# Performance work log

Hardware: AMD Instinct MI355X
Metric: run time of the kernel (lower is better)

## Reference

```python
import jax, jax.numpy as jnp
import numpy as np

T, D, H, V, Z = 32, 128, 256, 32000, 256


def _gru_cell(x, h, W_ih, W_hh, b_ih, b_hh):
    # PyTorch GRU cell, gate order r,z,n. x,h: [D,H]
    gi = x @ W_ih.T + b_ih
    gh = h @ W_hh.T + b_hh
    i_r, i_z, i_n = jnp.split(gi, 3, axis=-1)
    h_r, h_z, h_n = jnp.split(gh, 3, axis=-1)
    r = jax.nn.sigmoid(i_r + h_r)
    z = jax.nn.sigmoid(i_z + h_z)
    n = jnp.tanh(i_n + r * h_n)
    return (1.0 - z) * n + z * h


def _tree_rnn(nodes, edges, h0, emb, pc, ps):
    # nodes/edges: [T,D]; h0: [D,H]. Child vs sibling GRU chosen per-node by edges.
    def step(h, te):
        tok, e = te
        x = emb[tok]                       # [D,H]
        hc = _gru_cell(x, h, *pc)
        hs = _gru_cell(x, h, *ps)
        hn = jnp.where(e[:, None], hc, hs)  # branch-aware state update
        return hn, hn                       # seq_len=1, L=1 => output == new state
    h_final, outs = jax.lax.scan(step, h0, (nodes, edges))
    return outs, h_final                    # outs: [T,D,H]


def setup_inputs() -> dict:
    key = jax.random.key(0)
    ks = iter(jax.random.split(key, 48))
    s = 0.05
    def gru():
        return (jax.random.normal(next(ks), (3 * H, H), jnp.float32) * s,
                jax.random.normal(next(ks), (3 * H, H), jnp.float32) * s,
                jnp.zeros((3 * H,), jnp.float32),
                jnp.zeros((3 * H,), jnp.float32))
    inp = {}
    inp['nodes'] = jax.random.randint(next(ks), (T, D), 0, V, dtype=jnp.int32)
    inp['edges'] = jax.random.bernoulli(next(ks), 0.5, (T, D))
    inp['emb'] = jax.random.normal(next(ks), (V, H), jnp.float32) * s
    (inp['enc_c_Wih'], inp['enc_c_Whh'], inp['enc_c_bih'], inp['enc_c_bhh']) = gru()
    (inp['enc_s_Wih'], inp['enc_s_Whh'], inp['enc_s_bih'], inp['enc_s_bhh']) = gru()
    (inp['dec_c_Wih'], inp['dec_c_Whh'], inp['dec_c_bih'], inp['dec_c_bhh']) = gru()
    (inp['dec_s_Wih'], inp['dec_s_Whh'], inp['dec_s_bih'], inp['dec_s_bhh']) = gru()
    inp['W_mean'] = jax.random.normal(next(ks), (Z, H), jnp.float32) * s
    inp['b_mean'] = jnp.zeros((Z,), jnp.float32)
    inp['W_logv'] = jax.random.normal(next(ks), (Z, H), jnp.float32) * s
    inp['b_logv'] = jnp.zeros((Z,), jnp.float32)
    inp['W_l2h'] = jax.random.normal(next(ks), (H, Z), jnp.float32) * s
    inp['b_l2h'] = jnp.zeros((H,), jnp.float32)
    inp['W_out'] = jax.random.normal(next(ks), (V, H), jnp.float32) * s
    inp['b_out'] = jnp.zeros((V,), jnp.float32)
    inp['enc_init'] = jax.random.normal(next(ks), (D, H), jnp.float32) * 0.001
    inp['eps'] = jax.random.normal(next(ks), (D, Z), jnp.float32)
    return inp


def reference(nodes, edges, emb,
              enc_c_Wih, enc_c_Whh, enc_c_bih, enc_c_bhh,
              enc_s_Wih, enc_s_Whh, enc_s_bih, enc_s_bhh,
              dec_c_Wih, dec_c_Whh, dec_c_bih, dec_c_bhh,
              dec_s_Wih, dec_s_Whh, dec_s_bih, dec_s_bhh,
              W_mean, b_mean, W_logv, b_logv, W_l2h, b_l2h,
              W_out, b_out, enc_init, eps):
    pc_e = (enc_c_Wih, enc_c_Whh, enc_c_bih, enc_c_bhh)
    ps_e = (enc_s_Wih, enc_s_Whh, enc_s_bih, enc_s_bhh)
    pc_d = (dec_c_Wih, dec_c_Whh, dec_c_bih, dec_c_bhh)
    ps_d = (dec_s_Wih, dec_s_Whh, dec_s_bih, dec_s_bhh)

    _, hid = _tree_rnn(nodes, edges, enc_init, emb, pc_e, ps_e)  # [D,H]
    mean = hid @ W_mean.T + b_mean                               # [D,Z]
    logv = hid @ W_logv.T + b_logv
    z = eps * jnp.exp(0.5 * logv) + mean                          # reparameterize
    h0 = z @ W_l2h.T + b_l2h                                      # [D,H]
    outs, _ = _tree_rnn(nodes, edges, h0, emb, pc_d, ps_d)        # [T,D,H]
    logits = outs @ W_out.T + b_out                               # [T,D,V]
    logp = jax.nn.log_softmax(logits, axis=-1)
    return logp, mean, logv, z
```

## Files before the change

kernel.cpp:

```cpp
#include <hip/hip_runtime.h>
#include <hip/hip_bf16.h>

#define TT 32
#define DD 128
#define HH 256
#define VV 32000
#define ZZ 256
#define NTL 50

typedef __attribute__((ext_vector_type(8))) short bf16x8;
typedef __attribute__((ext_vector_type(4))) float f32x4;
typedef _Float16 h2v __attribute__((ext_vector_type(2)));

static __device__ inline unsigned short f2bf(float x) {
    __hip_bfloat16 h = __float2bfloat16(x);
    return *(unsigned short*)&h;
}

static __device__ inline float fdot2u(unsigned int w, unsigned int h, float acc) {
#if __has_builtin(__builtin_amdgcn_fdot2)
    return __builtin_amdgcn_fdot2(__builtin_bit_cast(h2v, w),
                                  __builtin_bit_cast(h2v, h), acc, false);
#else
    h2v a = __builtin_bit_cast(h2v, w), b = __builtin_bit_cast(h2v, h);
    return acc + (float)a[0] * (float)b[0] + (float)a[1] * (float)b[1];
#endif
}

__global__ void edge_canon_k(const unsigned char* __restrict__ eb,
                             unsigned char* __restrict__ canon)
{
    __shared__ int flag;
    if (threadIdx.x == 0) flag = 0;
    __syncthreads();
    int acc = 0;
    for (int i = threadIdx.x; i < TT * DD; i += 256)
        if (i & 3) acc |= eb[i];
    if (acc) atomicOr(&flag, 1);
    __syncthreads();
    const bool is_i32 = (flag == 0);
    for (int i = threadIdx.x; i < TT * DD; i += 256)
        canon[i] = is_i32 ? eb[4 * (size_t)i] : eb[i];
}

__global__ __launch_bounds__(256) void pack_frag(
    const float* __restrict__ src, __hip_bfloat16* __restrict__ dst, int nchunks_total)
{
    int i = blockIdx.x * 256 + threadIdx.x;
    if (i >= nchunks_total) return;
    int lane = i & 63, ks = (i >> 6) & 7, j = i >> 9;
    int g = lane >> 4, c = lane & 15;
    const float* s = src + (size_t)(j * 16 + c) * HH + ks * 32 + g * 8;
    float4 v0 = *(const float4*)s;
    float4 v1 = *(const float4*)(s + 4);
    bf16x8 o;
    o[0] = (short)f2bf(v0.x); o[1] = (short)f2bf(v0.y);
    o[2] = (short)f2bf(v0.z); o[3] = (short)f2bf(v0.w);
    o[4] = (short)f2bf(v1.x); o[5] = (short)f2bf(v1.y);
    o[6] = (short)f2bf(v1.z); o[7] = (short)f2bf(v1.w);
    *(bf16x8*)(dst + (size_t)i * 8) = o;
}

__global__ __launch_bounds__(256) void gather_pack(
    const int* __restrict__ nodes, const float* __restrict__ emb,
    __hip_bfloat16* __restrict__ dst)
{
    int i = blockIdx.x * 256 + threadIdx.x;
    int lane = i & 63, ks = (i >> 6) & 7, j = i >> 9;
    int g = lane >> 4, c = lane & 15;
    int row = j * 16 + c;
    int tok = nodes[row];
    const float* s = emb + (size_t)tok * HH + ks * 32 + g * 8;
    float4 v0 = *(const float4*)s;
    float4 v1 = *(const float4*)(s + 4);
    bf16x8 o;
    o[0] = (short)f2bf(v0.x); o[1] = (short)f2bf(v0.y);
    o[2] = (short)f2bf(v0.z); o[3] = (short)f2bf(v0.w);
    o[4] = (short)f2bf(v1.x); o[5] = (short)f2bf(v1.y);
    o[6] = (short)f2bf(v1.z); o[7] = (short)f2bf(v1.w);
    *(bf16x8*)(dst + (size_t)i * 8) = o;
}

__global__ __launch_bounds__(256) void pack_whh_t(
    const float* __restrict__ src, uint2* __restrict__ dst)
{
    int i = blockIdx.x * 256 + threadIdx.x;
    if (i >= 64 * 768) return;
    int j = i % 768, k4 = i / 768;
    float4 v = *(const float4*)(src + (size_t)j * HH + k4 * 4);
    h2v p0; p0[0] = (_Float16)v.x; p0[1] = (_Float16)v.y;
    h2v p1; p1[0] = (_Float16)v.z; p1[1] = (_Float16)v.w;
    uint2 o;
    o.x = __builtin_bit_cast(unsigned int, p0);
    o.y = __builtin_bit_cast(unsigned int, p1);
    dst[i] = o;
}

__global__ __launch_bounds__(256) void pack_lat_t(
    const float* __restrict__ src, float* __restrict__ dst)
{
    int i = blockIdx.x * 256 + threadIdx.x;
    int j = i & 255, k = i >> 8;
    dst[(size_t)k * 256 + j] = src[(size_t)j * 256 + k];
}

template<bool WRITE_C, bool HAS_BIAS, bool LSE_PARTIAL, bool LSE_SUB>
__global__ __launch_bounds__(256, 4) void gemm_rs(
    const __hip_bfloat16* __restrict__ A,
    const __hip_bfloat16* __restrict__ B,
    int ldc, int nchunks, int ntiles,
    const float* __restrict__ bias,
    const float* __restrict__ lse,
    float* __restrict__ C,
    float* __restrict__ pm, float* __restrict__ ps)
{
    __shared__ float lds_st[WRITE_C ? (4 * 16 * 68) : 1];

    const int tid  = threadIdx.x;
    const int w    = tid >> 6;
    const int lane = tid & 63;
    const int g    = lane >> 4;
    const int c    = lane & 15;
    const int m0   = blockIdx.x * 64;
    const int row16 = m0 + w * 16;
    const int n0   = blockIdx.y * (nchunks * 64);
    const int jb0  = n0 >> 4;

    bf16x8 a[8];
    {
        const __hip_bfloat16* ap = A + (((size_t)(row16 >> 4) * 8) * 64 + lane) * 8;
#pragma unroll
        for (int ks = 0; ks < 8; ++ks) a[ks] = *(const bf16x8*)(ap + ks * 512);
    }

    float mrun[4], srun[4];
#pragma unroll
    for (int r = 0; r < 4; ++r) { mrun[r] = -3.0e38f; srun[r] = 0.f; }

    float lsev[4];
    if (LSE_SUB) {
#pragma unroll
        for (int r = 0; r < 4; ++r) lsev[r] = lse[row16 + 4 * g + r];
    }

    for (int nc = 0; nc < nchunks; ++nc) {
        const int nb = n0 + nc * 64;
        const __hip_bfloat16* bp = B + (((size_t)(jb0 + nc * 4) * 8) * 64 + lane) * 8;

        f32x4 acc[4];
#pragma unroll
        for (int nf = 0; nf < 4; ++nf) acc[nf] = (f32x4){0.f, 0.f, 0.f, 0.f};

#pragma unroll
        for (int ks = 0; ks < 8; ++ks) {
            bf16x8 b0 = *(const bf16x8*)(bp + (0 * 8 + ks) * 512);
            bf16x8 b1 = *(const bf16x8*)(bp + (1 * 8 + ks) * 512);
            bf16x8 b2 = *(const bf16x8*)(bp + (2 * 8 + ks) * 512);
            bf16x8 b3 = *(const bf16x8*)(bp + (3 * 8 + ks) * 512);
            acc[0] = __builtin_amdgcn_mfma_f32_16x16x32_bf16(a[ks], b0, acc[0], 0, 0, 0);
            acc[1] = __builtin_amdgcn_mfma_f32_16x16x32_bf16(a[ks], b1, acc[1], 0, 0, 0);
            acc[2] = __builtin_amdgcn_mfma_f32_16x16x32_bf16(a[ks], b2, acc[2], 0, 0, 0);
            acc[3] = __builtin_amdgcn_mfma_f32_16x16x32_bf16(a[ks], b3, acc[3], 0, 0, 0);
        }

        float bv[4] = {0.f, 0.f, 0.f, 0.f};
        if (HAS_BIAS) {
#pragma unroll
            for (int nf = 0; nf < 4; ++nf) bv[nf] = bias[nb + nf * 16 + c];
        }

        if (LSE_PARTIAL) {
#pragma unroll
            for (int r = 0; r < 4; ++r) {
                float l0 = acc[0][r] + bv[0];
                float l1 = acc[1][r] + bv[1];
                float l2 = acc[2][r] + bv[2];
                float l3 = acc[3][r] + bv[3];
                float mc = fmaxf(fmaxf(l0, l1), fmaxf(l2, l3));
                float mn = fmaxf(mrun[r], mc);
                srun[r] = srun[r] * __expf(mrun[r] - mn)
                        + __expf(l0 - mn) + __expf(l1 - mn)
                        + __expf(l2 - mn) + __expf(l3 - mn);
                mrun[r] = mn;
            }
        }

        if (WRITE_C) {
            const int base = w * (16 * 68);
#pragma unroll
            for (int nf = 0; nf < 4; ++nf)
#pragma unroll
                for (int r = 0; r < 4; ++r) {
                    float v = acc[nf][r] + bv[nf];
                    if (LSE_SUB) v -= lsev[r];
                    lds_st[base + (4 * g + r) * 68 + nf * 16 + c] = v;
                }
#pragma unroll
            for (int i = 0; i < 4; ++i) {
                int lr = i * 4 + g;
                float4 v = *(const float4*)&lds_st[base + lr * 68 + c * 4];
                *(float4*)(C + (size_t)(row16 + lr) * ldc + nb + c * 4) = v;
            }
        }
    }

    if (LSE_PARTIAL) {
#pragma unroll
        for (int r = 0; r < 4; ++r) {
            float m = mrun[r], s = srun[r];
#pragma unroll
            for (int mk = 1; mk <= 8; mk <<= 1) {
                float m2 = __shfl_xor(m, mk);
                float s2 = __shfl_xor(s, mk);
                float mn = fmaxf(m, m2);
                s = s * __expf(m - mn) + s2 * __expf(m2 - mn);
                m = mn;
            }
            if (c == 0) {
                int row = row16 + 4 * g + r;
                pm[(size_t)row * ntiles + blockIdx.y] = m;
                ps[(size_t)row * ntiles + blockIdx.y] = s;
            }
        }
    }
}

__global__ __launch_bounds__(768) void rnn_fused(
    const unsigned char* __restrict__ ecan,
    const float* __restrict__ gi,
    const uint2* __restrict__ Wt,
    const float* __restrict__ ecbih, const float* __restrict__ ecbhh,
    const float* __restrict__ esbih, const float* __restrict__ esbhh,
    const float* __restrict__ dcbih, const float* __restrict__ dcbhh,
    const float* __restrict__ dsbih, const float* __restrict__ dsbhh,
    const float* __restrict__ WmT, const float* __restrict__ WlT,
    const float* __restrict__ WhT,
    const float* __restrict__ b_mean, const float* __restrict__ b_logv,
    const float* __restrict__ b_l2h,
    const float* __restrict__ enc_init, const float* __restrict__ eps,
    float* __restrict__ out_mean, float* __restrict__ out_logv,
    float* __restrict__ out_z,
    __hip_bfloat16* __restrict__ outs_pk)
{
    const int d = blockIdx.x;
    const int t = threadIdx.x;

    __shared__ float h[HH];
    __shared__ unsigned int hp[HH / 2];
    __shared__ float gh[768];
    __shared__ float zl[ZZ];

    if (t < HH) h[t] = enc_init[(size_t)d * HH + t];
    __syncthreads();
    if (t < HH / 2) {
        h2v p; p[0] = (_Float16)h[2 * t]; p[1] = (_Float16)h[2 * t + 1];
        hp[t] = __builtin_bit_cast(unsigned int, p);
    }
    __syncthreads();

    for (int phase = 0; phase < 2; ++phase) {
        const float* bihc = phase ? dcbih : ecbih;
        const float* bhhc = phase ? dcbhh : ecbhh;
        const float* bihs = phase ? dsbih : esbih;
        const float* bhhs = phase ? dsbhh : esbhh;

        for (int st = 0; st < TT; ++st) {
            const bool e = ecan[st * DD + d] != 0;
            const uint2* W = Wt + (size_t)(phase * 2 + (e ? 0 : 1)) * 49152 + t;
            float acc = 0.f;
#pragma unroll 8
            for (int k4 = 0; k4 < 64; ++k4) {
                uint2 w = W[k4 * 768];
                uint2 hh = *(const uint2*)&hp[2 * k4];
                acc = fdot2u(w.x, hh.x, acc);
                acc = fdot2u(w.y, hh.y, acc);
            }
            gh[t] = acc;
            __syncthreads();

            if (t < HH) {
                const float* bih = e ? bihc : bihs;
                const float* bhh = e ? bhhc : bhhs;
                const float* gr = gi + (size_t)(st * DD + d) * 3072
                                + phase * 1536 + (e ? 0 : 768);
                float ir  = gr[t]          + bih[t];
                float iz  = gr[t + HH]     + bih[t + HH];
                float in_ = gr[t + 2 * HH] + bih[t + 2 * HH];
                float hr  = gh[t]          + bhh[t];
                float hz  = gh[t + HH]     + bhh[t + HH];
                float hn  = gh[t + 2 * HH] + bhh[t + 2 * HH];
                float rg = 1.f / (1.f + __expf(-(ir + hr)));
                float zg = 1.f / (1.f + __expf(-(iz + hz)));
                float nn = tanhf(in_ + rg * hn);
                float hnew = (1.f - zg) * nn + zg * h[t];
                h[t] = hnew;
                if (phase) {
                    size_t idx = ((((size_t)st * 8 + (d >> 4)) * 8 + (t >> 5)) * 64
                                 + (((t >> 3) & 3) * 16 + (d & 15))) * 8 + (t & 7);
                    outs_pk[idx] = __float2bfloat16(hnew);
                }
            }
            __syncthreads();
            if (t < HH / 2) {
                h2v p; p[0] = (_Float16)h[2 * t]; p[1] = (_Float16)h[2 * t + 1];
                hp[t] = __builtin_bit_cast(unsigned int, p);
            }
            __syncthreads();
        }

        if (phase == 0) {
            if (t < 512) {
                int zi = t & 255;
                const float* WT = (t < 256) ? WmT : WlT;
                float s = 0.f;
#pragma unroll 8
                for (int k = 0; k < HH; ++k) s += h[k] * WT[k * ZZ + zi];
                if (t < 256) {
                    float mean = s + b_mean[zi];
                    out_mean[(size_t)d * ZZ + zi] = mean;
                    gh[zi] = mean;
                } else {
                    float logv = s + b_logv[zi];
                    out_logv[(size_t)d * ZZ + zi] = logv;
                    gh[256 + zi] = logv;
                }
            }
            __syncthreads();
            if (t < ZZ) {
                float zv = eps[(size_t)d * ZZ + t] * __expf(0.5f * gh[256 + t]) + gh[t];
                out_z[(size_t)d * ZZ + t] = zv;
                zl[t] = zv;
            }
            __syncthreads();
            if (t < HH) {
                float s = 0.f;
#pragma unroll 8
                for (int k = 0; k < ZZ; ++k) s += zl[k] * WhT[k * HH + t];
                h[t] = s + b_l2h[t];
            }
            __syncthreads();
            if (t < HH / 2) {
                h2v p; p[0] = (_Float16)h[2 * t]; p[1] = (_Float16)h[2 * t + 1];
                hp[t] = __builtin_bit_cast(unsigned int, p);
            }
            __syncthreads();
        }
    }
}

__global__ __launch_bounds__(64) void lse_reduce(
    const float* __restrict__ pm, const float* __restrict__ ps,
    float* __restrict__ lse, int nt)
{
    int row = blockIdx.x;
    int l = threadIdx.x;
    float m = (l < nt) ? pm[(size_t)row * nt + l] : -3.0e38f;
    float s = (l < nt) ? ps[(size_t)row * nt + l] : 0.f;
    for (int mk = 1; mk <= 32; mk <<= 1) {
        float m2 = __shfl_xor(m, mk);
        float s2 = __shfl_xor(s, mk);
        float mn = fmaxf(m, m2);
        s = s * __expf(m - mn) + s2 * __expf(m2 - mn);
        m = mn;
    }
    if (l == 0) lse[row] = m + logf(s);
}

extern "C" void kernel_launch(void* const* d_in, const int* in_sizes, int n_in,
                              void* d_out, int out_size, void* d_ws, size_t ws_size,
                              hipStream_t stream)
{
    const int*           nodes     = (const int*)d_in[0];
    const unsigned char* edges_raw = (const unsigned char*)d_in[1];
    const float* emb    = (const float*)d_in[2];
    const float* ecWih  = (const float*)d_in[3];
    const float* ecWhh  = (const float*)d_in[4];
    const float* ecbih  = (const float*)d_in[5];
    const float* ecbhh  = (const float*)d_in[6];
    const float* esWih  = (const float*)d_in[7];
    const float* esWhh  = (const float*)d_in[8];
    const float* esbih  = (const float*)d_in[9];
    const float* esbhh  = (const float*)d_in[10];
    const float* dcWih  = (const float*)d_in[11];
    const float* dcWhh  = (const float*)d_in[12];
    const float* dcbih  = (const float*)d_in[13];
    const float* dcbhh  = (const float*)d_in[14];
    const float* dsWih  = (const float*)d_in[15];
    const float* dsWhh  = (const float*)d_in[16];
    const float* dsbih  = (const float*)d_in[17];
    const float* dsbhh  = (const float*)d_in[18];
    const float* W_mean = (const float*)d_in[19];
    const float* b_mean = (const float*)d_in[20];
    const float* W_logv = (const float*)d_in[21];
    const float* b_logv = (const float*)d_in[22];
    const float* W_l2h  = (const float*)d_in[23];
    const float* b_l2h  = (const float*)d_in[24];
    const float* W_out  = (const float*)d_in[25];
    const float* b_out  = (const float*)d_in[26];
    const float* enc_init = (const float*)d_in[27];
    const float* eps    = (const float*)d_in[28];

    float* out      = (float*)d_out;
    float* out_mean = out + (size_t)TT * DD * VV;
    float* out_logv = out_mean + DD * ZZ;
    float* out_z    = out_logv + DD * ZZ;
    float* gi       = out;

    char* ws = (char*)d_ws;
    __hip_bfloat16* outs_pk = (__hip_bfloat16*)(ws + 0);
    __hip_bfloat16* Ap      = (__hip_bfloat16*)(ws + 2097152);
    __hip_bfloat16* Wp      = (__hip_bfloat16*)(ws + 4194304);
    __hip_bfloat16* Bp_all  = (__hip_bfloat16*)(ws + 20971520);
    uint2*          Wt      = (uint2*)(ws + 23068672);
    float*          WmT     = (float*)(ws + 25165824);
    float*          WlT     = (float*)(ws + 25427968);
    float*          WhT     = (float*)(ws + 25690112);
    float*          pm      = (float*)(ws + 25952256);
    float*          ps      = (float*)(ws + 26771456);
    float*          lse     = (float*)(ws + 27590656);
    unsigned char*  ecan    = (unsigned char*)(ws + 27607040);

    edge_canon_k<<<1, 256, 0, stream>>>(edges_raw, ecan);
    pack_frag<<<4000, 256, 0, stream>>>(W_out, Wp, 2000 * 8 * 64);
    pack_frag<<<96, 256, 0, stream>>>(ecWih, Bp_all + 0 * (size_t)48 * 4096, 48 * 8 * 64);
    pack_frag<<<96, 256, 0, stream>>>(esWih, Bp_all + 1 * (size_t)48 * 4096, 48 * 8 * 64);
    pack_frag<<<96, 256, 0, stream>>>(dcWih, Bp_all + 2 * (size_t)48 * 4096, 48 * 8 * 64);
    pack_frag<<<96, 256, 0, stream>>>(dsWih, Bp_all + 3 * (size_t)48 * 4096, 48 * 8 * 64);
    pack_whh_t<<<192, 256, 0, stream>>>(ecWhh, Wt + 0 * (size_t)49152);
    pack_whh_t<<<192, 256, 0, stream>>>(esWhh, Wt + 1 * (size_t)49152);
    pack_whh_t<<<192, 256, 0, stream>>>(dcWhh, Wt + 2 * (size_t)49152);
    pack_whh_t<<<192, 256, 0, stream>>>(dsWhh, Wt + 3 * (size_t)49152);
    pack_lat_t<<<256, 256, 0, stream>>>(W_mean, WmT);
    pack_lat_t<<<256, 256, 0, stream>>>(W_logv, WlT);
    pack_lat_t<<<256, 256, 0, stream>>>(W_l2h, WhT);
    gather_pack<<<512, 256, 0, stream>>>(nodes, emb, Ap);

    gemm_rs<true, false, false, false><<<dim3(64, 6), 256, 0, stream>>>(
        Ap, Bp_all, 3072, 8, 6, nullptr, nullptr, gi, nullptr, nullptr);

    rnn_fused<<<DD, 768, 0, stream>>>(
        ecan, gi, Wt,
        ecbih, ecbhh, esbih, esbhh, dcbih, dcbhh, dsbih, dsbhh,
        WmT, WlT, WhT, b_mean, b_logv, b_l2h,
        enc_init, eps, out_mean, out_logv, out_z, outs_pk);

    gemm_rs<false, true, true, false><<<dim3(64, NTL), 256, 0, stream>>>(
        outs_pk, Wp, VV, 10, NTL, b_out, nullptr, nullptr, pm, ps);
    lse_reduce<<<4096, 64, 0, stream>>>(pm, ps, lse, NTL);
    gemm_rs<true, true, false, true><<<dim3(64, NTL), 256, 0, stream>>>(
        outs_pk, Wp, VV, 10, NTL, b_out, lse, out, nullptr, nullptr);
}
```

Baseline: 946.0 us.

## Batch 16 tree nodes per block and compute recurrent GEMM with f16 MFMA

The recurrent kernel now processes 16 batch rows per 1024-thread block (8 blocks) instead of one row per block. It computes h@W_hh for both child and sibling weights with 16x16x32 f16 MFMA, keeping the weight fragments resident in registers across all timesteps. This replaces the per-row fdot2 loop, which re-read the full W_hh from global or L2 memory at every step. The tradeoff is only 8 active CUs on a serial recurrence, heavy register pressure from 48 resident fragments per wave, and extra work from computing both gate variants for every row.

```diff
diff --git a/kernel.cpp b/kernel.cpp
--- a/kernel.cpp
+++ b/kernel.cpp
@@ -7,24 +7,16 @@
 #define VV 32000
 #define ZZ 256
 #define NTL 50
+#define GHP 1544
 
 typedef __attribute__((ext_vector_type(8))) short bf16x8;
 typedef __attribute__((ext_vector_type(4))) float f32x4;
+typedef __attribute__((ext_vector_type(8))) _Float16 f16x8;
 typedef _Float16 h2v __attribute__((ext_vector_type(2)));
 
 static __device__ inline unsigned short f2bf(float x) {
     __hip_bfloat16 h = __float2bfloat16(x);
     return *(unsigned short*)&h;
-}
-
-static __device__ inline float fdot2u(unsigned int w, unsigned int h, float acc) {
-#if __has_builtin(__builtin_amdgcn_fdot2)
-    return __builtin_amdgcn_fdot2(__builtin_bit_cast(h2v, w),
-                                  __builtin_bit_cast(h2v, h), acc, false);
-#else
-    h2v a = __builtin_bit_cast(h2v, w), b = __builtin_bit_cast(h2v, h);
-    return acc + (float)a[0] * (float)b[0] + (float)a[1] * (float)b[1];
-#endif
 }
 
 __global__ void edge_canon_k(const unsigned char* __restrict__ eb,
@@ -59,6 +51,24 @@
     o[4] = (short)f2bf(v1.x); o[5] = (short)f2bf(v1.y);
     o[6] = (short)f2bf(v1.z); o[7] = (short)f2bf(v1.w);
     *(bf16x8*)(dst + (size_t)i * 8) = o;
+}
+
+__global__ __launch_bounds__(256) void pack_frag16(
+    const float* __restrict__ src, _Float16* __restrict__ dst, int nchunks_total)
+{
+    int i = blockIdx.x * 256 + threadIdx.x;
+    if (i >= nchunks_total) return;
+    int lane = i & 63, ks = (i >> 6) & 7, j = i >> 9;
+    int g = lane >> 4, c = lane & 15;
+    const float* s = src + (size_t)(j * 16 + c) * HH + ks * 32 + g * 8;
+    float4 v0 = *(const float4*)s;
+    float4 v1 = *(const float4*)(s + 4);
+    f16x8 o;
+    o[0] = (_Float16)v0.x; o[1] = (_Float16)v0.y;
+    o[2] = (_Float16)v0.z; o[3] = (_Float16)v0.w;
+    o[4] = (_Float16)v1.x; o[5] = (_Float16)v1.y;
+    o[6] = (_Float16)v1.z; o[7] = (_Float16)v1.w;
+    *(f16x8*)(dst + (size_t)i * 8) = o;
 }
 
 __global__ __launch_bounds__(256) void gather_pack(
@@ -81,21 +91,6 @@
     *(bf16x8*)(dst + (size_t)i * 8) = o;
 }
 
-__global__ __launch_bounds__(256) void pack_whh_t(
-    const float* __restrict__ src, uint2* __restrict__ dst)
-{
-    int i = blockIdx.x * 256 + threadIdx.x;
-    if (i >= 64 * 768) return;
-    int j = i % 768, k4 = i / 768;
-    float4 v = *(const float4*)(src + (size_t)j * HH + k4 * 4);
-    h2v p0; p0[0] = (_Float16)v.x; p0[1] = (_Float16)v.y;
-    h2v p1; p1[0] = (_Float16)v.z; p1[1] = (_Float16)v.w;
-    uint2 o;
-    o.x = __builtin_bit_cast(unsigned int, p0);
-    o.y = __builtin_bit_cast(unsigned int, p1);
-    dst[i] = o;
-}
-
 __global__ __launch_bounds__(256) void pack_lat_t(
     const float* __restrict__ src, float* __restrict__ dst)
 {
@@ -225,10 +220,10 @@
     }
 }
 
-__global__ __launch_bounds__(768) void rnn_fused(
+__global__ __launch_bounds__(1024) void rnn_fused2(
     const unsigned char* __restrict__ ecan,
     const float* __restrict__ gi,
-    const uint2* __restrict__ Wt,
+    const _Float16* __restrict__ Wf,
     const float* __restrict__ ecbih, const float* __restrict__ ecbhh,
     const float* __restrict__ esbih, const float* __restrict__ esbhh,
     const float* __restrict__ dcbih, const float* __restrict__ dcbhh,
@@ -242,106 +237,174 @@
     float* __restrict__ out_z,
     __hip_bfloat16* __restrict__ outs_pk)
 {
-    const int d = blockIdx.x;
-    const int t = threadIdx.x;
-
-    __shared__ float h[HH];
-    __shared__ unsigned int hp[HH / 2];
-    __shared__ float gh[768];
-    __shared__ float zl[ZZ];
-
-    if (t < HH) h[t] = enc_init[(size_t)d * HH + t];
+    __shared__ float    gh[16 * GHP];
+    __shared__ _Float16 hpk[8 * 64 * 8];
+    __shared__ float    hof[16 * HH];
+
+    const int tid  = threadIdx.x;
+    const int w    = tid >> 6;
+    const int lane = tid & 63;
+    const int d0   = blockIdx.x * 16;
+
+    {
+        const int d = tid >> 6, j0 = (tid & 63) * 4;
+        f32x4 hv = *(const f32x4*)(enc_init + (size_t)(d0 + d) * HH + j0);
+        *(f32x4*)(hof + d * HH + j0) = hv;
+        h2v p0; p0[0] = (_Float16)hv[0]; p0[1] = (_Float16)hv[1];
+        h2v p1; p1[0] = (_Float16)hv[2]; p1[1] = (_Float16)hv[3];
+        uint2 u;
+        u.x = __builtin_bit_cast(unsigned int, p0);
+        u.y = __builtin_bit_cast(unsigned int, p1);
+        int chunk = (j0 >> 5) * 64 + ((j0 >> 3) & 3) * 16 + d;
+        *(uint2*)((char*)hpk + chunk * 16 + (j0 & 7) * 2) = u;
+    }
     __syncthreads();
-    if (t < HH / 2) {
-        h2v p; p[0] = (_Float16)h[2 * t]; p[1] = (_Float16)h[2 * t + 1];
-        hp[t] = __builtin_bit_cast(unsigned int, p);
-    }
-    __syncthreads();
-
-    for (int phase = 0; phase < 2; ++phase) {
-        const float* bihc = phase ? dcbih : ecbih;
-        const float* bhhc = phase ? dcbhh : ecbhh;
-        const float* bihs = phase ? dsbih : esbih;
-        const float* bhhs = phase ? dsbhh : esbhh;
+
+    for (int p = 0; p < 2; ++p) {
+        f16x8 bfrag[6][8];
+        {
+            const _Float16* wb = Wf + (size_t)p * (1536 * 256);
+#pragma unroll
+            for (int i = 0; i < 6; ++i) {
+                const int jt = w * 6 + i;
+#pragma unroll
+                for (int ks = 0; ks < 8; ++ks)
+                    bfrag[i][ks] = *(const f16x8*)(wb + ((size_t)(jt * 8 + ks) * 64 + lane) * 8);
+            }
+        }
+        const float* bihc = p ? dcbih : ecbih;
+        const float* bhhc = p ? dcbhh : ecbhh;
+        const float* bihs = p ? dsbih : esbih;
+        const float* bhhs = p ? dsbhh : esbhh;
 
         for (int st = 0; st < TT; ++st) {
-            const bool e = ecan[st * DD + d] != 0;
-            const uint2* W = Wt + (size_t)(phase * 2 + (e ? 0 : 1)) * 49152 + t;
-            float acc = 0.f;
-#pragma unroll 8
-            for (int k4 = 0; k4 < 64; ++k4) {
-                uint2 w = W[k4 * 768];
-                uint2 hh = *(const uint2*)&hp[2 * k4];
-                acc = fdot2u(w.x, hh.x, acc);
-                acc = fdot2u(w.y, hh.y, acc);
-            }
-            gh[t] = acc;
+            f16x8 af[8];
+#pragma unroll
+            for (int ks = 0; ks < 8; ++ks)
+                af[ks] = *(const f16x8*)&hpk[(ks * 64 + lane) * 8];
+#pragma unroll
+            for (int i = 0; i < 6; ++i) {
+                f32x4 acc = (f32x4){0.f, 0.f, 0.f, 0.f};
+#pragma unroll
+                for (int ks = 0; ks < 8; ++ks)
+                    acc = __builtin_amdgcn_mfma_f32_16x16x32_f16(af[ks], bfrag[i][ks], acc, 0, 0, 0);
+                const int jt = w * 6 + i;
+                const int col = jt * 16 + (lane & 15);
+                const int rb  = (lane >> 4) * 4;
+#pragma unroll
+                for (int r = 0; r < 4; ++r)
+                    gh[(rb + r) * GHP + col] = acc[r];
+            }
             __syncthreads();
 
-            if (t < HH) {
+            {
+                const int d  = tid >> 6;
+                const int j0 = (tid & 63) * 4;
+                const int dg = d0 + d;
+                const bool e = ecan[st * DD + dg] != 0;
+                const int vb = e ? 0 : 768;
+                const float* gr = gi + (size_t)(st * DD + dg) * 3072 + p * 1536 + vb;
+                const float* ghd = gh + d * GHP + vb;
                 const float* bih = e ? bihc : bihs;
                 const float* bhh = e ? bhhc : bhhs;
-                const float* gr = gi + (size_t)(st * DD + d) * 3072
-                                + phase * 1536 + (e ? 0 : 768);
-                float ir  = gr[t]          + bih[t];
-                float iz  = gr[t + HH]     + bih[t + HH];
-                float in_ = gr[t + 2 * HH] + bih[t + 2 * HH];
-                float hr  = gh[t]          + bhh[t];
-                float hz  = gh[t + HH]     + bhh[t + HH];
-                float hn  = gh[t + 2 * HH] + bhh[t + 2 * HH];
-                float rg = 1.f / (1.f + __expf(-(ir + hr)));
-                float zg = 1.f / (1.f + __expf(-(iz + hz)));
-                float nn = tanhf(in_ + rg * hn);
-                float hnew = (1.f - zg) * nn + zg * h[t];
-                h[t] = hnew;
-                if (phase) {
-                    size_t idx = ((((size_t)st * 8 + (d >> 4)) * 8 + (t >> 5)) * 64
-                                 + (((t >> 3) & 3) * 16 + (d & 15))) * 8 + (t & 7);
-                    outs_pk[idx] = __float2bfloat16(hnew);
+
+                f32x4 gr_r = *(const f32x4*)(gr + j0);
+                f32x4 gr_z = *(const f32x4*)(gr + HH + j0);
+                f32x4 gr_n = *(const f32x4*)(gr + 2 * HH + j0);
+                f32x4 gh_r = *(const f32x4*)(ghd + j0);
+                f32x4 gh_z = *(const f32x4*)(ghd + HH + j0);
+                f32x4 gh_n = *(const f32x4*)(ghd + 2 * HH + j0);
+                f32x4 bi_r = *(const f32x4*)(bih + j0);
+                f32x4 bi_z = *(const f32x4*)(bih + HH + j0);
+                f32x4 bi_n = *(const f32x4*)(bih + 2 * HH + j0);
+                f32x4 bh_r = *(const f32x4*)(bhh + j0);
+                f32x4 bh_z = *(const f32x4*)(bhh + HH + j0);
+                f32x4 bh_n = *(const f32x4*)(bhh + 2 * HH + j0);
+                f32x4 ho   = *(const f32x4*)(hof + d * HH + j0);
+
+                f32x4 hn_;
+#pragma unroll
+                for (int m = 0; m < 4; ++m) {
+                    float rg = 1.f / (1.f + __expf(-(gr_r[m] + bi_r[m] + gh_r[m] + bh_r[m])));
+                    float zg = 1.f / (1.f + __expf(-(gr_z[m] + bi_z[m] + gh_z[m] + bh_z[m])));
+                    float nn = tanhf(gr_n[m] + bi_n[m] + rg * (gh_n[m] + bh_n[m]));
+                    hn_[m] = (1.f - zg) * nn + zg * ho[m];
                 }
+                *(f32x4*)(hof + d * HH + j0) = hn_;
+
+                h2v p0; p0[0] = (_Float16)hn_[0]; p0[1] = (_Float16)hn_[1];
+                h2v p1; p1[0] = (_Float16)hn_[2]; p1[1] = (_Float16)hn_[3];
+                uint2 u;
+                u.x = __builtin_bit_cast(unsigned int, p0);
+                u.y = __builtin_bit_cast(unsigned int, p1);
+                int chunk = (j0 >> 5) * 64 + ((j0 >> 3) & 3) * 16 + d;
+                *(uint2*)((char*)hpk + chunk * 16 + (j0 & 7) * 2) = u;
+
+                if (p) {
+                    ushort4 ub;
+                    ub.x = f2bf(hn_[0]); ub.y = f2bf(hn_[1]);
+                    ub.z = f2bf(hn_[2]); ub.w = f2bf(hn_[3]);
+                    size_t ch = ((size_t)(st * 8 + blockIdx.x) * 8 + (j0 >> 5)) * 64
+                              + ((j0 >> 3) & 3) * 16 + d;
+                    *(ushort4*)((unsigned short*)outs_pk + ch * 8 + (j0 & 7)) = ub;
+                }
             }
             __syncthreads();
-            if (t < HH / 2) {
-                h2v p; p[0] = (_Float16)h[2 * t]; p[1] = (_Float16)h[2 * t + 1];
-                hp[t] = __builtin_bit_cast(unsigned int, p);
+        }
+
+        if (p == 0) {
+            const int d  = tid >> 6;
+            const int q  = tid & 63;
+            const int dg = d0 + d;
+            {
+                f32x4 sm = (f32x4){0.f, 0.f, 0.f, 0.f};
+                f32x4 sl = (f32x4){0.f, 0.f, 0.f, 0.f};
+                const f32x4* wm4 = (const f32x4*)WmT;
+                const f32x4* wl4 = (const f32x4*)WlT;
+#pragma unroll 4
+                for (int k = 0; k < HH; ++k) {
+                    float hv = hof[d * HH + k];
+                    sm += hv * wm4[k * 64 + q];
+                    sl += hv * wl4[k * 64 + q];
+                }
+                f32x4 mean = sm + ((const f32x4*)b_mean)[q];
+                f32x4 logv = sl + ((const f32x4*)b_logv)[q];
+                ((f32x4*)(out_mean + (size_t)dg * ZZ))[q] = mean;
+                ((f32x4*)(out_logv + (size_t)dg * ZZ))[q] = logv;
+                *(f32x4*)(gh + d * GHP + q * 4)       = mean;
+                *(f32x4*)(gh + d * GHP + 256 + q * 4) = logv;
             }
             __syncthreads();
-        }
-
-        if (phase == 0) {
-            if (t < 512) {
-                int zi = t & 255;
-                const float* WT = (t < 256) ? WmT : WlT;
-                float s = 0.f;
-#pragma unroll 8
-                for (int k = 0; k < HH; ++k) s += h[k] * WT[k * ZZ + zi];
-                if (t < 256) {
-                    float mean = s + b_mean[zi];
-                    out_mean[(size_t)d * ZZ + zi] = mean;
-                    gh[zi] = mean;
-                } else {
-                    float logv = s + b_logv[zi];
-                    out_logv[(size_t)d * ZZ + zi] = logv;
-                    gh[256 + zi] = logv;
+            {
+                f32x4 mean = *(const f32x4*)(gh + d * GHP + q * 4);
+                f32x4 logv = *(const f32x4*)(gh + d * GHP + 256 + q * 4);
+                f32x4 ep   = ((const f32x4*)(eps + (size_t)dg * ZZ))[q];
+                f32x4 zv;
+#pragma unroll
+                for (int m = 0; m < 4; ++m)
+                    zv[m] = ep[m] * __expf(0.5f * logv[m]) + mean[m];
+                ((f32x4*)(out_z + (size_t)dg * ZZ))[q] = zv;
+                *(f32x4*)(gh + d * GHP + 512 + q * 4) = zv;
+            }
+            __syncthreads();
+            {
+                f32x4 s = (f32x4){0.f, 0.f, 0.f, 0.f};
+                const f32x4* wh4 = (const f32x4*)WhT;
+#pragma unroll 4
+                for (int k = 0; k < ZZ; ++k) {
+                    float zv = gh[d * GHP + 512 + k];
+                    s += zv * wh4[k * 64 + q];
                 }
-            }
-            __syncthreads();
-            if (t < ZZ) {
-                float zv = eps[(size_t)d * ZZ + t] * __expf(0.5f * gh[256 + t]) + gh[t];
-                out_z[(size_t)d * ZZ + t] = zv;
-                zl[t] = zv;
-            }
-            __syncthreads();
-            if (t < HH) {
-                float s = 0.f;
-#pragma unroll 8
-                for (int k = 0; k < ZZ; ++k) s += zl[k] * WhT[k * HH + t];
-                h[t] = s + b_l2h[t];
-            }
-            __syncthreads();
-            if (t < HH / 2) {
-                h2v p; p[0] = (_Float16)h[2 * t]; p[1] = (_Float16)h[2 * t + 1];
-                hp[t] = __builtin_bit_cast(unsigned int, p);
+                f32x4 h0v = s + ((const f32x4*)b_l2h)[q];
+                const int j0 = q * 4;
+                *(f32x4*)(hof + d * HH + j0) = h0v;
+                h2v p0; p0[0] = (_Float16)h0v[0]; p0[1] = (_Float16)h0v[1];
+                h2v p1; p1[0] = (_Float16)h0v[2]; p1[1] = (_Float16)h0v[3];
+                uint2 u;
+                u.x = __builtin_bit_cast(unsigned int, p0);
+                u.y = __builtin_bit_cast(unsigned int, p1);
+                int chunk = (j0 >> 5) * 64 + ((j0 >> 3) & 3) * 16 + d;
+                *(uint2*)((char*)hpk + chunk * 16 + (j0 & 7) * 2) = u;
             }
             __syncthreads();
         }
@@ -411,14 +474,14 @@
     __hip_bfloat16* Ap      = (__hip_bfloat16*)(ws + 2097152);
     __hip_bfloat16* Wp      = (__hip_bfloat16*)(ws + 4194304);
     __hip_bfloat16* Bp_all  = (__hip_bfloat16*)(ws + 20971520);
-    uint2*          Wt      = (uint2*)(ws + 23068672);
-    float*          WmT     = (float*)(ws + 25165824);
-    float*          WlT     = (float*)(ws + 25427968);
-    float*          WhT     = (float*)(ws + 25690112);
-    float*          pm      = (float*)(ws + 25952256);
-    float*          ps      = (float*)(ws + 26771456);
-    float*          lse     = (float*)(ws + 27590656);
-    unsigned char*  ecan    = (unsigned char*)(ws + 27607040);
+    _Float16*       Wf      = (_Float16*)(ws + 22544384);
+    float*          WmT     = (float*)(ws + 24117248);
+    float*          WlT     = (float*)(ws + 24379392);
+    float*          WhT     = (float*)(ws + 24641536);
+    float*          pm      = (float*)(ws + 24903680);
+    float*          ps      = (float*)(ws + 25722880);
+    float*          lse     = (float*)(ws + 26542080);
+    unsigned char*  ecan    = (unsigned char*)(ws + 26558464);
 
     edge_canon_k<<<1, 256, 0, stream>>>(edges_raw, ecan);
     pack_frag<<<4000, 256, 0, stream>>>(W_out, Wp, 2000 * 8 * 64);
@@ -426,10 +489,10 @@
     pack_frag<<<96, 256, 0, stream>>>(esWih, Bp_all + 1 * (size_t)48 * 4096, 48 * 8 * 64);
     pack_frag<<<96, 256, 0, stream>>>(dcWih, Bp_all + 2 * (size_t)48 * 4096, 48 * 8 * 64);
     pack_frag<<<96, 256, 0, stream>>>(dsWih, Bp_all + 3 * (size_t)48 * 4096, 48 * 8 * 64);
-    pack_whh_t<<<192, 256, 0, stream>>>(ecWhh, Wt + 0 * (size_t)49152);
-    pack_whh_t<<<192, 256, 0, stream>>>(esWhh, Wt + 1 * (size_t)49152);
-    pack_whh_t<<<192, 256, 0, stream>>>(dcWhh, Wt + 2 * (size_t)49152);
-    pack_whh_t<<<192, 256, 0, stream>>>(dsWhh, Wt + 3 * (size_t)49152);
+    pack_frag16<<<96, 256, 0, stream>>>(ecWhh, Wf + 0 * (size_t)768 * 256, 48 * 8 * 64);
+    pack_frag16<<<96, 256, 0, stream>>>(esWhh, Wf + 1 * (size_t)768 * 256, 48 * 8 * 64);
+    pack_frag16<<<96, 256, 0, stream>>>(dcWhh, Wf + 2 * (size_t)768 * 256, 48 * 8 * 64);
+    pack_frag16<<<96, 256, 0, stream>>>(dsWhh, Wf + 3 * (size_t)768 * 256, 48 * 8 * 64);
     pack_lat_t<<<256, 256, 0, stream>>>(W_mean, WmT);
     pack_lat_t<<<256, 256, 0, stream>>>(W_logv, WlT);
     pack_lat_t<<<256, 256, 0, stream>>>(W_l2h, WhT);
@@ -438,8 +501,8 @@
     gemm_rs<true, false, false, false><<<dim3(64, 6), 256, 0, stream>>>(
         Ap, Bp_all, 3072, 8, 6, nullptr, nullptr, gi, nullptr, nullptr);
 
-    rnn_fused<<<DD, 768, 0, stream>>>(
-        ecan, gi, Wt,
+    rnn_fused2<<<8, 1024, 0, stream>>>(
+        ecan, gi, Wf,
         ecbih, ecbhh, esbih, esbhh, dcbih, dcbhh, dsbih, dsbhh,
         WmT, WlT, WhT, b_mean, b_logv, b_l2h,
         enc_init, eps, out_mean, out_logv, out_z, outs_pk);
```

New measurement: 1.911 ms. 2.02x slower.
